# Optimization experiments

Hardware: AMD Instinct MI355X
Metric: run time of the kernel (lower is better)

The kernel has to match this reference:

```python
import jax, jax.numpy as jnp
import numpy as np

B, T, D, H, WIN, G = 2, 2048, 768, 12, 16, 32
HD = D // H            # 64
K = 2 * WIN + 1        # local kernel size = 33


def setup_inputs() -> dict:
    key = jax.random.key(0)
    ks = jax.random.split(key, 5)
    s = 1.0 / np.sqrt(D).astype(np.float32)
    x = jax.random.normal(ks[0], (B, T, D), jnp.float32)
    # first G tokens of every batch are global (matches original's nonzero(global_mask[b]))
    global_mask = jnp.zeros((B, T), jnp.int32).at[:, :G].set(1)
    Wq = jax.random.normal(ks[1], (D, D), jnp.float32) * s
    Wk = jax.random.normal(ks[2], (D, D), jnp.float32) * s
    Wv = jax.random.normal(ks[3], (D, D), jnp.float32) * s
    Wo = jax.random.normal(ks[4], (D, D), jnp.float32) * s
    bq = jnp.zeros((D,), jnp.float32)
    bk = jnp.zeros((D,), jnp.float32)
    bv = jnp.zeros((D,), jnp.float32)
    bo = jnp.zeros((D,), jnp.float32)
    return {"x": x, "global_mask": global_mask, "Wq": Wq, "bq": bq,
            "Wk": Wk, "bk": bk, "Wv": Wv, "bv": bv, "Wo": Wo, "bo": bo}


def reference(x, global_mask, Wq, bq, Wk, bk, Wv, bv, Wo, bo):
    def split_heads(y):
        return y.reshape(B, T, H, HD).transpose(0, 2, 1, 3)  # [B,H,T,HD]

    q = split_heads(x @ Wq + bq)
    k = split_heads(x @ Wk + bk)
    v = split_heads(x @ Wv + bv)

    scale = 1.0 / np.sqrt(HD).astype(np.float32)

    offs = jnp.arange(-WIN, WIN + 1)
    idx = jnp.arange(T)[:, None] + offs[None, :]          # [T,K]
    valid = (idx >= 0) & (idx < T)                        # [T,K]
    idxc = jnp.clip(idx, 0, T - 1)

    k_loc = k[:, :, idxc]                                 # [B,H,T,K,HD]
    s_loc = jnp.einsum('bhtd,bhtkd->bhtk', q, k_loc) * scale
    s_loc = jnp.where(valid, s_loc, -jnp.inf)             # out-of-range excluded from softmax

    # global tokens (same positions for every batch by construction)
    g_idx = jnp.nonzero(global_mask[0], size=G)[0]        # [G]
    k_g = k[:, :, g_idx]                                  # [B,H,G,HD]
    v_g = v[:, :, g_idx]
    s_g = jnp.einsum('bhtd,bhgd->bhtg', q, k_g) * scale   # [B,H,T,G]

    # joint softmax over [local window, global tokens] (globals in window are double-counted,
    # exactly as in the original torch.cat([local_s, g_score]))
    attn = jax.nn.softmax(jnp.concatenate([s_loc, s_g], axis=-1), axis=-1)
    a_loc = jnp.where(valid, attn[..., :K], 0.0)          # [B,H,T,K]
    a_g = attn[..., K:]                                   # [B,H,T,G]

    v_loc = v[:, :, idxc]                                 # [B,H,T,K,HD]
    ctx = (jnp.einsum('bhtk,bhtkd->bhtd', a_loc, v_loc)
           + jnp.einsum('bhtg,bhgd->bhtd', a_g, v_g))     # [B,H,T,HD]

    out = ctx.transpose(0, 2, 1, 3).reshape(B, T, D) @ Wo + bo

    # dense attention map: scatter local band (add; invalid entries are 0),
    # then overwrite global columns (matches original write order)
    rows = jnp.arange(T)[:, None]                         # [T,1]
    full_attn = jnp.zeros((B, H, T, T), jnp.float32)
    full_attn = full_attn.at[:, :, rows, idxc].add(a_loc)
    full_attn = full_attn.at[:, :, :, g_idx].set(a_g)
    return out, full_attn
```

## Files before the change

### kernel.cpp

```cpp
#include <hip/hip_runtime.h>

typedef unsigned short u16;
typedef __attribute__((ext_vector_type(4))) u16 u16x4;
typedef __attribute__((ext_vector_type(8))) u16 u16x8;
typedef __attribute__((ext_vector_type(8))) short bf16x8;
typedef __attribute__((ext_vector_type(4))) float f32x4;

#define BB 2
#define TT 2048
#define DD 768
#define NH 12
#define HDIM 64
#define NQKV 2304
#define MM 4096

__device__ __forceinline__ u16 f2bf(float f) {
  unsigned u = __float_as_uint(f);
  u += 0x7fffu + ((u >> 16) & 1u);
  return (u16)(u >> 16);
}
__device__ __forceinline__ float bf2f(u16 s) {
  return __uint_as_float(((unsigned)s) << 16);
}
__device__ __forceinline__ void async_load16(const void* g, void* l) {
  __builtin_amdgcn_global_load_lds((const __attribute__((address_space(1))) void*)g,
                                   (__attribute__((address_space(3))) void*)l, 16, 0, 0);
}

__global__ __launch_bounds__(256) void prep_all(const float* __restrict__ x,
                                                const float* __restrict__ Wq, const float* __restrict__ Wk,
                                                const float* __restrict__ Wv, const float* __restrict__ Wo,
                                                const int* __restrict__ gm,
                                                const float* __restrict__ bq, const float* __restrict__ bk,
                                                const float* __restrict__ bv,
                                                u16* __restrict__ xb, u16* __restrict__ wqkvT,
                                                u16* __restrict__ woT,
                                                int* __restrict__ gidx, float* __restrict__ biasqkv) {
  __shared__ float tile[32][33];
  const int bid = blockIdx.x;
  const int tid = threadIdx.x;
  if (bid < 3072) {
    int i = bid * 256 + tid;
    float4 v = ((const float4*)x)[i];
    u16x4 o = { f2bf(v.x), f2bf(v.y), f2bf(v.z), f2bf(v.w) };
    ((u16x4*)xb)[i] = o;
  } else if (bid < 5376) {
    int r = bid - 3072;
    int z = r / 576; r %= 576;
    int kx = r % 24, ny = r / 24;
    const float* W = (z == 0) ? Wq : (z == 1) ? Wk : (z == 2) ? Wv : Wo;
    u16* dst = (z < 3) ? (wqkvT + (size_t)z * DD * DD) : woT;
    int k0 = kx * 32, n0 = ny * 32;
    int tx = tid & 31, ty = tid >> 5;
#pragma unroll
    for (int j = 0; j < 4; ++j)
      tile[ty + j * 8][tx] = W[(size_t)(k0 + ty + j * 8) * DD + n0 + tx];
    __syncthreads();
#pragma unroll
    for (int j = 0; j < 4; ++j)
      dst[(size_t)(n0 + ty + j * 8) * DD + k0 + tx] = f2bf(tile[tx][ty + j * 8]);
  } else {
    for (int n = tid; n < NQKV; n += 256)
      biasqkv[n] = (n < 768) ? bq[n] : (n < 1536) ? bk[n - 768] : bv[n - 1536];
    if (tid < 64) {
      int lane = tid;
      if (lane < 32) gidx[lane] = 0;
      int base = 0;
      for (int c0 = 0; c0 < TT; c0 += 64) {
        int mval = gm[c0 + lane];
        unsigned long long bal = __ballot(mval != 0);
        int pre = __popcll(bal & ((1ull << lane) - 1ull));
        if (mval && (base + pre) < 32) gidx[base + pre] = c0 + lane;
        base += __popcll(bal);
        if (base >= 32) break;
      }
    }
  }
}

__global__ __launch_bounds__(256) void gemm_qkv(const u16* __restrict__ A, const u16* __restrict__ BT,
                                                const float* __restrict__ bias, u16* __restrict__ C,
                                                int Ndim, int Kd) {
  __shared__ __attribute__((aligned(16))) u16 As[128 * 64];
  __shared__ __attribute__((aligned(16))) u16 Bs[128 * 64];
  const int tid = threadIdx.x;
  const int wave = tid >> 6, lane = tid & 63;
  const int m0 = blockIdx.x * 128, n0 = blockIdx.y * 128;
  const int wm = (wave & 1) << 6, wn = (wave >> 1) << 6;
  const int lr = lane & 15, lk = lane >> 4;
  const int srow_b = lane >> 3;
  const int scol = (lane & 7) * 8;

  f32x4 acc[4][4] = {};

  const int kIters = Kd >> 6;
  for (int kt = 0; kt < kIters; ++kt) {
#pragma unroll
    for (int cc = 0; cc < 4; ++cc) {
      int c = wave * 4 + cc;
      int srow = c * 8 + srow_b;
      async_load16(A + (size_t)(m0 + srow) * Kd + (kt << 6) + scol, (void*)(As + c * 512));
      async_load16(BT + (size_t)(n0 + srow) * Kd + (kt << 6) + scol, (void*)(Bs + c * 512));
    }
    __syncthreads();
#pragma unroll
    for (int kc = 0; kc < 2; ++kc) {
      bf16x8 af[4], bfr[4];
#pragma unroll
      for (int i = 0; i < 4; ++i)
        af[i] = *(const bf16x8*)(As + (wm + i * 16 + lr) * 64 + kc * 32 + lk * 8);
#pragma unroll
      for (int j = 0; j < 4; ++j)
        bfr[j] = *(const bf16x8*)(Bs + (wn + j * 16 + lr) * 64 + kc * 32 + lk * 8);
#pragma unroll
      for (int i = 0; i < 4; ++i)
#pragma unroll
        for (int j = 0; j < 4; ++j)
          acc[i][j] = __builtin_amdgcn_mfma_f32_16x16x32_bf16(af[i], bfr[j], acc[i][j], 0, 0, 0);
    }
    __syncthreads();
  }

#pragma unroll
  for (int i = 0; i < 4; ++i) {
    const int row = m0 + wm + i * 16 + lk * 4;
#pragma unroll
    for (int j = 0; j < 4; ++j) {
      const int col = n0 + wn + j * 16 + lr;
      const float bs = bias[col];
#pragma unroll
      for (int r = 0; r < 4; ++r)
        C[(size_t)(row + r) * Ndim + col] = f2bf(acc[i][j][r] + bs);
    }
  }
}

__global__ __launch_bounds__(256) void attn_kernel(const u16* __restrict__ qb,
                                                   const int* __restrict__ gidx,
                                                   u16* __restrict__ ctxb,
                                                   float* __restrict__ fattn) {
  __shared__ __attribute__((aligned(16))) u16 Kl[96 * 72];
  __shared__ __attribute__((aligned(16))) u16 Kg[32 * 72];
  __shared__ __attribute__((aligned(16))) u16 Vl[96 * 72];
  __shared__ __attribute__((aligned(16))) u16 Vg[32 * 72];
  __shared__ __attribute__((aligned(16))) float probs[64 * 66];
  __shared__ int gidxs[32];

  const int tid = threadIdx.x;
  const int blk = blockIdx.x;
  const int chunk = blk & 31;
  const int h = (blk >> 5) % NH;
  const int b = blk / 384;
  const int t0 = chunk << 6;

  {
    const int r = tid >> 3;
    const int c8 = (tid & 7) << 3;
#pragma unroll
    for (int it = 0; it < 3; ++it) {
      int rr = it * 32 + r;
      int t = t0 - 16 + rr;
      t = t < 0 ? 0 : (t > TT - 1 ? TT - 1 : t);
      const u16* src = qb + (size_t)(b * TT + t) * NQKV + h * HDIM + c8;
      *(u16x8*)(Kl + rr * 72 + c8) = *(const u16x8*)(src + 768);
      *(u16x8*)(Vl + rr * 72 + c8) = *(const u16x8*)(src + 1536);
    }
    {
      int t = gidx[r];
      const u16* src = qb + (size_t)(b * TT + t) * NQKV + h * HDIM + c8;
      *(u16x8*)(Kg + r * 72 + c8) = *(const u16x8*)(src + 768);
      *(u16x8*)(Vg + r * 72 + c8) = *(const u16x8*)(src + 1536);
    }
    if (tid < 32) gidxs[tid] = gidx[tid];
  }
  __syncthreads();

  const int tl = tid >> 2, sub = tid & 3;
  const int t = t0 + tl;
  const u16* qp = qb + (size_t)(b * TT + t) * NQKV + h * HDIM;
  u16x8 qpk[8];
#pragma unroll
  for (int i = 0; i < 8; ++i) qpk[i] = *(const u16x8*)(qp + i * 8);

  float sc[17];
  float mmax = -__builtin_inff();
#pragma unroll
  for (int i = 0; i < 17; ++i) {
    const int s = sub + (i << 2);
    const u16* kp;
    bool valid;
    if (s < 33) { kp = Kl + (tl + s) * 72; int j = t - 16 + s; valid = (j >= 0) && (j < TT); }
    else if (s < 65) { kp = Kg + (s - 33) * 72; valid = true; }
    else { kp = Kg; valid = false; }
    float d = 0.f;
#pragma unroll
    for (int i2 = 0; i2 < 8; ++i2) {
      u16x8 kv = *(const u16x8*)(kp + i2 * 8);
      u16x8 qq = qpk[i2];
#pragma unroll
      for (int e = 0; e < 8; ++e) d += bf2f(qq[e]) * bf2f(kv[e]);
    }
    sc[i] = valid ? d * 0.125f : -__builtin_inff();
    mmax = fmaxf(mmax, sc[i]);
  }
  mmax = fmaxf(mmax, __shfl_xor(mmax, 1));
  mmax = fmaxf(mmax, __shfl_xor(mmax, 2));
  float sum = 0.f;
#pragma unroll
  for (int i = 0; i < 17; ++i) { sc[i] = __expf(sc[i] - mmax); sum += sc[i]; }
  sum += __shfl_xor(sum, 1);
  sum += __shfl_xor(sum, 2);
  const float inv = 1.0f / sum;
#pragma unroll
  for (int i = 0; i < 17; ++i) {
    const int s = sub + (i << 2);
    sc[i] *= inv;
    if (s < 65) probs[tl * 66 + s] = sc[i];
  }
  __syncthreads();

  float cacc[16];
#pragma unroll
  for (int i = 0; i < 16; ++i) cacc[i] = 0.f;
#pragma unroll 1
  for (int k = 0; k < 65; ++k) {
    const float pv = probs[tl * 66 + k];
    const u16* vp = (k < 33) ? (Vl + (tl + k) * 72) : (Vg + (k - 33) * 72);
    const u16* vq = vp + (sub << 4);
    u16x8 v0 = *(const u16x8*)(vq);
    u16x8 v1 = *(const u16x8*)(vq + 8);
#pragma unroll
    for (int e = 0; e < 8; ++e) { cacc[e] += pv * bf2f(v0[e]); cacc[8 + e] += pv * bf2f(v1[e]); }
  }
  {
    u16x8 cb0, cb1;
#pragma unroll
    for (int e = 0; e < 8; ++e) { cb0[e] = f2bf(cacc[e]); cb1[e] = f2bf(cacc[8 + e]); }
    u16* dst = ctxb + (size_t)(b * TT + t) * DD + h * HDIM + (sub << 4);
    *(u16x8*)dst = cb0;
    *(u16x8*)(dst + 8) = cb1;
  }

  float* fbase = fattn + ((size_t)(b * NH + h) * TT + t0) * TT;
#pragma unroll 2
  for (int it = 0; it < 128; ++it) {
    int q = it * 256 + tid;
    int rl = q >> 9;
    int c4 = (q & 511) << 2;
    int trow = t0 + rl;
    f32x4 v = {0.f, 0.f, 0.f, 0.f};
    int kk = c4 - trow + 16;
    if (kk >= -3 && kk < 33) {
#pragma unroll
      for (int e = 0; e < 4; ++e) {
        int k2 = kk + e;
        if ((unsigned)k2 < 33u) v[e] = probs[rl * 66 + k2];
      }
    }
    __builtin_nontemporal_store(v, (f32x4*)(fbase + (size_t)rl * TT + c4));
  }
  __syncthreads();
#pragma unroll
  for (int rep = 0; rep < 8; ++rep) {
    int w = rep * 256 + tid;
    int rl = w >> 5, g = w & 31;
    fbase[(size_t)rl * TT + gidxs[g]] = probs[rl * 66 + 33 + g];
  }
}

__global__ __launch_bounds__(256) void gemm_out(const u16* __restrict__ ctxb, const u16* __restrict__ woT,
                                                const float* __restrict__ bo, float* __restrict__ out) {
  __shared__ __attribute__((aligned(16))) u16 sA[64 * 64];
  __shared__ __attribute__((aligned(16))) u16 sB[128 * 64];
  const int tid = threadIdx.x;
  const int bid = blockIdx.x;
  const int wave = tid >> 6, lane = tid & 63;
  const int m0 = (bid & 63) * 64, n0 = (bid >> 6) * 128;
  const int wn = wave << 5;
  const int lr = lane & 15, lk = lane >> 4;
  const int srow_b = lane >> 3;
  const int scol = (lane & 7) * 8;

  f32x4 acc[4][2] = {};
  for (int kt = 0; kt < DD / 64; ++kt) {
#pragma unroll
    for (int cc = 0; cc < 2; ++cc) {
      int c = wave * 2 + cc;
      int srow = c * 8 + srow_b;
      async_load16(ctxb + (size_t)(m0 + srow) * DD + (kt << 6) + scol, (void*)(sA + c * 512));
    }
#pragma unroll
    for (int cc = 0; cc < 4; ++cc) {
      int c = wave * 4 + cc;
      int srow = c * 8 + srow_b;
      async_load16(woT + (size_t)(n0 + srow) * DD + (kt << 6) + scol, (void*)(sB + c * 512));
    }
    __syncthreads();
#pragma unroll
    for (int kc = 0; kc < 2; ++kc) {
      bf16x8 af[4], bfr[2];
#pragma unroll
      for (int i = 0; i < 4; ++i)
        af[i] = *(const bf16x8*)(sA + (i * 16 + lr) * 64 + kc * 32 + lk * 8);
#pragma unroll
      for (int j = 0; j < 2; ++j)
        bfr[j] = *(const bf16x8*)(sB + (wn + j * 16 + lr) * 64 + kc * 32 + lk * 8);
#pragma unroll
      for (int i = 0; i < 4; ++i)
#pragma unroll
        for (int j = 0; j < 2; ++j)
          acc[i][j] = __builtin_amdgcn_mfma_f32_16x16x32_bf16(af[i], bfr[j], acc[i][j], 0, 0, 0);
    }
    __syncthreads();
  }
#pragma unroll
  for (int i = 0; i < 4; ++i) {
    const int row = m0 + i * 16 + lk * 4;
#pragma unroll
    for (int j = 0; j < 2; ++j) {
      const int col = n0 + wn + j * 16 + lr;
      const float bs = bo[col];
#pragma unroll
      for (int r = 0; r < 4; ++r)
        out[(size_t)(row + r) * DD + col] = acc[i][j][r] + bs;
    }
  }
}

extern "C" void kernel_launch(void* const* d_in, const int* in_sizes, int n_in,
                              void* d_out, int out_size, void* d_ws, size_t ws_size,
                              hipStream_t stream) {
  const float* x  = (const float*)d_in[0];
  const int* gm   = (const int*)d_in[1];
  const float* Wq = (const float*)d_in[2];
  const float* bq = (const float*)d_in[3];
  const float* Wk = (const float*)d_in[4];
  const float* bk = (const float*)d_in[5];
  const float* Wv = (const float*)d_in[6];
  const float* bv = (const float*)d_in[7];
  const float* Wo = (const float*)d_in[8];
  const float* bo = (const float*)d_in[9];

  float* out = (float*)d_out;
  float* fattn = out + (size_t)BB * TT * DD;

  char* p = (char*)d_ws;
  u16* xb      = (u16*)p;  p += (size_t)MM * DD * 2;
  u16* wqkvT   = (u16*)p;  p += (size_t)NQKV * DD * 2;
  u16* woT     = (u16*)p;  p += (size_t)DD * DD * 2;
  float* biasq = (float*)p; p += (size_t)NQKV * 4;
  int* gidx    = (int*)p;  p += 128;
  u16* qkvb    = (u16*)p;  p += (size_t)MM * NQKV * 2;
  u16* ctxb    = (u16*)p;  p += (size_t)MM * DD * 2;

  prep_all<<<5377, 256, 0, stream>>>(x, Wq, Wk, Wv, Wo, gm, bq, bk, bv,
                                     xb, wqkvT, woT, gidx, biasq);
  gemm_qkv<<<dim3(MM / 128, NQKV / 128), 256, 0, stream>>>(xb, wqkvT, biasq, qkvb, NQKV, DD);
  attn_kernel<<<BB * NH * (TT / 64), 256, 0, stream>>>(qkvb, gidx, ctxb, fattn);
  gemm_out<<<384, 256, 0, stream>>>(ctxb, woT, bo, out);
}
```

Before: 533.0 us.

## Zero the dense attention map off-band inside the QKV GEMM launch

Adds 768 extra blocks to the QKV GEMM launch. They write zeros to every column of the dense T×T attention map outside each row's local band, so the large zero-fill overlaps with GEMM compute instead of running inside the attention kernel. The attention kernel now writes only the roughly ten float4 chunks per row that cover the band, then overwrites the global columns as before. This puts memory-bound zero traffic alongside the compute-bound GEMM, at the cost of more scheduling pressure on the GEMM blocks and an ordering dependency on the band boundaries.

```diff
diff --git a/kernel.cpp b/kernel.cpp
--- a/kernel.cpp
+++ b/kernel.cpp
@@ -78,14 +78,41 @@
   }
 }
 
+#define ZSTREAM_BLOCKS 768
 __global__ __launch_bounds__(256) void gemm_qkv(const u16* __restrict__ A, const u16* __restrict__ BT,
                                                 const float* __restrict__ bias, u16* __restrict__ C,
+                                                float* __restrict__ fattn,
                                                 int Ndim, int Kd) {
+  const int tid = threadIdx.x;
+  const int gid = blockIdx.x;
+
+  if (gid < ZSTREAM_BLOCKS) {
+    const int chunk = gid & 31;
+    const int h = (gid >> 5) % NH;
+    const int b = gid / 384;
+    const int t0 = chunk << 6;
+    float* fbase = fattn + ((size_t)(b * NH + h) * TT + t0) * TT;
+    const f32x4 z = {0.f, 0.f, 0.f, 0.f};
+#pragma unroll 2
+    for (int it = 0; it < 128; ++it) {
+      int q = it * 256 + tid;
+      int rl = q >> 9;
+      int j = q & 511;
+      int t = t0 + rl;
+      int bl4 = (t >= 16) ? ((t - 16) >> 2) : 0;
+      int th = t + 16; if (th > TT - 1) th = TT - 1;
+      int bh4 = th >> 2;
+      if (j < bl4 || j > bh4)
+        __builtin_nontemporal_store(z, (f32x4*)(fbase + (size_t)rl * TT + (j << 2)));
+    }
+    return;
+  }
+
   __shared__ __attribute__((aligned(16))) u16 As[128 * 64];
   __shared__ __attribute__((aligned(16))) u16 Bs[128 * 64];
-  const int tid = threadIdx.x;
+  const int bid = gid - ZSTREAM_BLOCKS;
   const int wave = tid >> 6, lane = tid & 63;
-  const int m0 = blockIdx.x * 128, n0 = blockIdx.y * 128;
+  const int m0 = (bid & 31) << 7, n0 = (bid >> 5) << 7;
   const int wm = (wave & 1) << 6, wn = (wave >> 1) << 6;
   const int lr = lane & 15, lk = lane >> 4;
   const int srow_b = lane >> 3;
@@ -242,22 +269,24 @@
   }
 
   float* fbase = fattn + ((size_t)(b * NH + h) * TT + t0) * TT;
-#pragma unroll 2
-  for (int it = 0; it < 128; ++it) {
-    int q = it * 256 + tid;
-    int rl = q >> 9;
-    int c4 = (q & 511) << 2;
-    int trow = t0 + rl;
-    f32x4 v = {0.f, 0.f, 0.f, 0.f};
-    int kk = c4 - trow + 16;
-    if (kk >= -3 && kk < 33) {
+#pragma unroll 1
+  for (int w = tid; w < 640; w += 256) {
+    int rl = w / 10, jj = w - rl * 10;
+    int tr = t0 + rl;
+    int bl4 = (tr >= 16) ? ((tr - 16) >> 2) : 0;
+    int th = tr + 16; if (th > TT - 1) th = TT - 1;
+    int bh4 = th >> 2;
+    int j = bl4 + jj;
+    if (j <= bh4) {
+      f32x4 v;
 #pragma unroll
       for (int e = 0; e < 4; ++e) {
-        int k2 = kk + e;
-        if ((unsigned)k2 < 33u) v[e] = probs[rl * 66 + k2];
+        int c = (j << 2) + e;
+        int k = c - tr + 16;
+        v[e] = ((unsigned)k < 33u) ? probs[rl * 66 + k] : 0.f;
       }
-    }
-    __builtin_nontemporal_store(v, (f32x4*)(fbase + (size_t)rl * TT + c4));
+      *(f32x4*)(fbase + (size_t)rl * TT + (j << 2)) = v;
+    }
   }
   __syncthreads();
 #pragma unroll
@@ -355,7 +384,8 @@
 
   prep_all<<<5377, 256, 0, stream>>>(x, Wq, Wk, Wv, Wo, gm, bq, bk, bv,
                                      xb, wqkvT, woT, gidx, biasq);
-  gemm_qkv<<<dim3(MM / 128, NQKV / 128), 256, 0, stream>>>(xb, wqkvT, biasq, qkvb, NQKV, DD);
+  gemm_qkv<<<ZSTREAM_BLOCKS + (MM / 128) * (NQKV / 128), 256, 0, stream>>>(
+      xb, wqkvT, biasq, qkvb, fattn, NQKV, DD);
   attn_kernel<<<BB * NH * (TT / 64), 256, 0, stream>>>(qkvb, gidx, ctxb, fattn);
   gemm_out<<<384, 256, 0, stream>>>(ctxb, woT, bo, out);
 }
```

Measured after the change: 557.0 us. 1.05x slower.

## Interleave zero-fill stores of attention map with score and context compute

Applied to the files above, without the earlier changes.

The zero portion of the dense attention map, everything outside each row's band, is now written from inside the score loop and the PV accumulation loop. Those stores are spread across iterations so they overlap with arithmetic instead of running as one long store tail. The band region is written afterwards as a separate small pass that reads the probabilities from shared memory. This adds per-iteration index and branch work, and it depends on the two store sets covering every column of every row exactly once.

```diff
diff --git a/kernel.cpp b/kernel.cpp
--- a/kernel.cpp
+++ b/kernel.cpp
@@ -153,6 +153,23 @@
   const int b = blk / 384;
   const int t0 = chunk << 6;
 
+  float* fbase = fattn + ((size_t)(b * NH + h) * TT + t0) * TT;
+  const f32x4 z4 = {0.f, 0.f, 0.f, 0.f};
+
+#define EMIT_ZERO(qslot)                                                     \
+  {                                                                          \
+    int q_ = (qslot);                                                        \
+    if (q_ < 32768) {                                                        \
+      int rl_ = q_ >> 9, j_ = q_ & 511;                                      \
+      int tr_ = t0 + rl_;                                                    \
+      int bl4_ = (tr_ >= 16) ? ((tr_ - 16) >> 2) : 0;                        \
+      int th_ = tr_ + 16; if (th_ > TT - 1) th_ = TT - 1;                    \
+      int bh4_ = th_ >> 2;                                                   \
+      if (j_ < bl4_ || j_ > bh4_)                                            \
+        __builtin_nontemporal_store(z4, (f32x4*)(fbase + (size_t)rl_ * TT + (j_ << 2))); \
+    }                                                                        \
+  }
+
   {
     const int r = tid >> 3;
     const int c8 = (tid & 7) << 3;
@@ -202,6 +219,8 @@
     }
     sc[i] = valid ? d * 0.125f : -__builtin_inff();
     mmax = fmaxf(mmax, sc[i]);
+    EMIT_ZERO((i * 2 + 0) * 256 + tid);
+    EMIT_ZERO((i * 2 + 1) * 256 + tid);
   }
   mmax = fmaxf(mmax, __shfl_xor(mmax, 1));
   mmax = fmaxf(mmax, __shfl_xor(mmax, 2));
@@ -231,6 +250,8 @@
     u16x8 v1 = *(const u16x8*)(vq + 8);
 #pragma unroll
     for (int e = 0; e < 8; ++e) { cacc[e] += pv * bf2f(v0[e]); cacc[8 + e] += pv * bf2f(v1[e]); }
+    EMIT_ZERO(8704 + (k * 2 + 0) * 256 + tid);
+    EMIT_ZERO(8704 + (k * 2 + 1) * 256 + tid);
   }
   {
     u16x8 cb0, cb1;
@@ -241,23 +262,24 @@
     *(u16x8*)(dst + 8) = cb1;
   }
 
-  float* fbase = fattn + ((size_t)(b * NH + h) * TT + t0) * TT;
-#pragma unroll 2
-  for (int it = 0; it < 128; ++it) {
-    int q = it * 256 + tid;
-    int rl = q >> 9;
-    int c4 = (q & 511) << 2;
-    int trow = t0 + rl;
-    f32x4 v = {0.f, 0.f, 0.f, 0.f};
-    int kk = c4 - trow + 16;
-    if (kk >= -3 && kk < 33) {
+#pragma unroll 1
+  for (int w = tid; w < 640; w += 256) {
+    int rl = w / 10, jj = w - rl * 10;
+    int tr = t0 + rl;
+    int bl4 = (tr >= 16) ? ((tr - 16) >> 2) : 0;
+    int th = tr + 16; if (th > TT - 1) th = TT - 1;
+    int bh4 = th >> 2;
+    int j = bl4 + jj;
+    if (j <= bh4) {
+      f32x4 v;
 #pragma unroll
       for (int e = 0; e < 4; ++e) {
-        int k2 = kk + e;
-        if ((unsigned)k2 < 33u) v[e] = probs[rl * 66 + k2];
+        int c = (j << 2) + e;
+        int k = c - tr + 16;
+        v[e] = ((unsigned)k < 33u) ? probs[rl * 66 + k] : 0.f;
       }
-    }
-    __builtin_nontemporal_store(v, (f32x4*)(fbase + (size_t)rl * TT + c4));
+      __builtin_nontemporal_store(v, (f32x4*)(fbase + (size_t)rl * TT + (j << 2)));
+    }
   }
   __syncthreads();
 #pragma unroll
@@ -266,6 +288,7 @@
     int rl = w >> 5, g = w & 31;
     fbase[(size_t)rl * TT + gidxs[g]] = probs[rl * 66 + 33 + g];
   }
+#undef EMIT_ZERO
 }
 
 __global__ __launch_bounds__(256) void gemm_out(const u16* __restrict__ ctxb, const u16* __restrict__ woT,
```

Result: no change. 541.7 us (+1.6%).

## Split attention-map zero fill around compute to overlap stores with attention math

Applied to the files above, without the earlier changes.

The dense attention-map write is split in two. Out-of-band zero tiles are stored without waiting on probabilities: part of them after the K/V shared-memory load and the rest after the PV accumulation. Each thread writes its own row's band tiles straight from its softmax results. This interleaves the large write stream with the score and context compute, and it drops the barrier between softmax and the band write. The added index logic per store and a more complex write pattern could cost some efficiency.

```diff
diff --git a/kernel.cpp b/kernel.cpp
--- a/kernel.cpp
+++ b/kernel.cpp
@@ -153,27 +153,20 @@
   const int b = blk / 384;
   const int t0 = chunk << 6;
 
-  {
-    const int r = tid >> 3;
-    const int c8 = (tid & 7) << 3;
-#pragma unroll
-    for (int it = 0; it < 3; ++it) {
-      int rr = it * 32 + r;
-      int t = t0 - 16 + rr;
-      t = t < 0 ? 0 : (t > TT - 1 ? TT - 1 : t);
-      const u16* src = qb + (size_t)(b * TT + t) * NQKV + h * HDIM + c8;
-      *(u16x8*)(Kl + rr * 72 + c8) = *(const u16x8*)(src + 768);
-      *(u16x8*)(Vl + rr * 72 + c8) = *(const u16x8*)(src + 1536);
-    }
-    {
-      int t = gidx[r];
-      const u16* src = qb + (size_t)(b * TT + t) * NQKV + h * HDIM + c8;
-      *(u16x8*)(Kg + r * 72 + c8) = *(const u16x8*)(src + 768);
-      *(u16x8*)(Vg + r * 72 + c8) = *(const u16x8*)(src + 1536);
-    }
-    if (tid < 32) gidxs[tid] = gidx[tid];
-  }
-  __syncthreads();
+  float* fbase = fattn + ((size_t)(b * NH + h) * TT + t0) * TT;
+  const f32x4 z4 = {0.f, 0.f, 0.f, 0.f};
+
+#define EMIT_ZERO(qslot)                                                     \
+  {                                                                          \
+    int q_ = (qslot);                                                        \
+    int rl_ = q_ >> 9, j_ = q_ & 511;                                        \
+    int tr_ = t0 + rl_;                                                      \
+    int bl4_ = (tr_ >= 16) ? ((tr_ - 16) >> 2) : 0;                          \
+    int th_ = tr_ + 16; if (th_ > TT - 1) th_ = TT - 1;                      \
+    int bh4_ = th_ >> 2;                                                     \
+    if (j_ < bl4_ || j_ > bh4_)                                              \
+      __builtin_nontemporal_store(z4, (f32x4*)(fbase + (size_t)rl_ * TT + (j_ << 2))); \
+  }
 
   const int tl = tid >> 2, sub = tid & 3;
   const int t = t0 + tl;
@@ -181,6 +174,31 @@
   u16x8 qpk[8];
 #pragma unroll
   for (int i = 0; i < 8; ++i) qpk[i] = *(const u16x8*)(qp + i * 8);
+
+  {
+    const int r = tid >> 3;
+    const int c8 = (tid & 7) << 3;
+#pragma unroll
+    for (int it = 0; it < 3; ++it) {
+      int rr = it * 32 + r;
+      int tt = t0 - 16 + rr;
+      tt = tt < 0 ? 0 : (tt > TT - 1 ? TT - 1 : tt);
+      const u16* src = qb + (size_t)(b * TT + tt) * NQKV + h * HDIM + c8;
+      *(u16x8*)(Kl + rr * 72 + c8) = *(const u16x8*)(src + 768);
+      *(u16x8*)(Vl + rr * 72 + c8) = *(const u16x8*)(src + 1536);
+    }
+    {
+      int tt = gidx[r];
+      const u16* src = qb + (size_t)(b * TT + tt) * NQKV + h * HDIM + c8;
+      *(u16x8*)(Kg + r * 72 + c8) = *(const u16x8*)(src + 768);
+      *(u16x8*)(Vg + r * 72 + c8) = *(const u16x8*)(src + 1536);
+    }
+    if (tid < 32) gidxs[tid] = gidx[tid];
+  }
+  __syncthreads();
+
+#pragma unroll 2
+  for (int it = 0; it < 56; ++it) EMIT_ZERO(it * 256 + tid);
 
   float sc[17];
   float mmax = -__builtin_inff();
@@ -217,7 +235,26 @@
     sc[i] *= inv;
     if (s < 65) probs[tl * 66 + s] = sc[i];
   }
-  __syncthreads();
+
+  {
+    int bl4 = (t >= 16) ? ((t - 16) >> 2) : 0;
+    int th = t + 16; if (th > TT - 1) th = TT - 1;
+    int bh4 = th >> 2;
+#pragma unroll
+    for (int r2 = 0; r2 < 3; ++r2) {
+      int j = bl4 + sub + (r2 << 2);
+      if (j <= bh4) {
+        f32x4 v;
+#pragma unroll
+        for (int e = 0; e < 4; ++e) {
+          int c = (j << 2) + e;
+          int k = c - t + 16;
+          v[e] = ((unsigned)k < 33u) ? probs[tl * 66 + k] : 0.f;
+        }
+        __builtin_nontemporal_store(v, (f32x4*)(fbase + (size_t)tl * TT + (j << 2)));
+      }
+    }
+  }
 
   float cacc[16];
 #pragma unroll
@@ -241,24 +278,9 @@
     *(u16x8*)(dst + 8) = cb1;
   }
 
-  float* fbase = fattn + ((size_t)(b * NH + h) * TT + t0) * TT;
 #pragma unroll 2
-  for (int it = 0; it < 128; ++it) {
-    int q = it * 256 + tid;
-    int rl = q >> 9;
-    int c4 = (q & 511) << 2;
-    int trow = t0 + rl;
-    f32x4 v = {0.f, 0.f, 0.f, 0.f};
-    int kk = c4 - trow + 16;
-    if (kk >= -3 && kk < 33) {
-#pragma unroll
-      for (int e = 0; e < 4; ++e) {
-        int k2 = kk + e;
-        if ((unsigned)k2 < 33u) v[e] = probs[rl * 66 + k2];
-      }
-    }
-    __builtin_nontemporal_store(v, (f32x4*)(fbase + (size_t)rl * TT + c4));
-  }
+  for (int it = 56; it < 128; ++it) EMIT_ZERO(it * 256 + tid);
+
   __syncthreads();
 #pragma unroll
   for (int rep = 0; rep < 8; ++rep) {
@@ -266,6 +288,7 @@
     int rl = w >> 5, g = w & 31;
     fbase[(size_t)rl * TT + gidxs[g]] = probs[rl * 66 + 33 + g];
   }
+#undef EMIT_ZERO
 }
 
 __global__ __launch_bounds__(256) void gemm_out(const u16* __restrict__ ctxb, const u16* __restrict__ woT,
```

New measurement: 527.2 us (median of 2 runs). About the same (-1.1%).
